# Performance work log

Measured on AMD Instinct MI355X. Metric: run time of the kernel, lower is better.

Reference implementation:

```python
import jax, jax.numpy as jnp
import numpy as np

N = 50000       # nodes
E = 800000      # edges (avg degree 16)
F_IN = 128      # num_node_features
H = 128         # hidden_dim
C = 16          # num_classes
G = 512         # graphs in batch


def setup_inputs() -> dict:
    key = jax.random.key(0)
    ks = jax.random.split(key, 12)
    x = jax.random.normal(ks[0], (N, F_IN), dtype=jnp.float32)
    edge_index = jax.random.randint(ks[1], (2, E), 0, N, dtype=jnp.int32)
    batch = jnp.sort(jax.random.randint(ks[2], (N,), 0, G, dtype=jnp.int32))
    def lin(k, fan_in, shape):
        bound = 1.0 / np.sqrt(fan_in)
        return jax.random.uniform(k, shape, jnp.float32, -bound, bound)
    # SAGEConv1: lin_l (aggr, with bias), lin_r (root, no bias)
    w1l = lin(ks[3], F_IN, (F_IN, H)); b1 = lin(ks[4], F_IN, (H,))
    w1r = lin(ks[5], F_IN, (F_IN, H))
    # SAGEConv2
    w2l = lin(ks[6], H, (H, H)); b2 = lin(ks[7], H, (H,))
    w2r = lin(ks[8], H, (H, H))
    # final fc
    wf = lin(ks[9], H, (H, C)); bf = lin(ks[10], H, (C,))
    return {"x": x, "edge_index": edge_index, "batch": batch,
            "w1l": w1l, "b1": b1, "w1r": w1r,
            "w2l": w2l, "b2": b2, "w2r": w2r,
            "wf": wf, "bf": bf}


def _sage_conv(x, src, dst, wl, bl, wr):
    # mean-aggregate source-node features at destination nodes
    msg_sum = jax.ops.segment_sum(x[src], dst, num_segments=N)      # [N, d]
    cnt = jax.ops.segment_sum(jnp.ones((src.shape[0], 1), x.dtype), dst,
                              num_segments=N)                        # [N, 1]
    aggr = msg_sum / jnp.maximum(cnt, 1.0)
    return aggr @ wl + bl + x @ wr


def reference(x, edge_index, batch, w1l, b1, w1r, w2l, b2, w2r, wf, bf):
    src, dst = edge_index[0], edge_index[1]
    h = jax.nn.relu(_sage_conv(x, src, dst, w1l, b1, w1r))
    # dropout(p=0.5) is identity at inference
    h = jax.nn.relu(_sage_conv(h, src, dst, w2l, b2, w2r))
    # global_mean_pool over graph ids
    gsum = jax.ops.segment_sum(h, batch, num_segments=G)             # [G, H]
    gcnt = jax.ops.segment_sum(jnp.ones((N, 1), h.dtype), batch,
                               num_segments=G)                        # [G, 1]
    g = gsum / jnp.maximum(gcnt, 1.0)
    logits = g @ wf + bf
    return jax.nn.log_softmax(logits, axis=1)
```

## Files before the change

### kernel.cpp

```cpp
#include <hip/hip_runtime.h>
#include <hip/hip_bf16.h>
#include <math.h>


#define FDIM 128

typedef __attribute__((ext_vector_type(8))) short bf16x8;
typedef __attribute__((ext_vector_type(4))) float f32x4;

__device__ inline unsigned short f2bf(float f) {
    union { float f; unsigned u; } v; v.f = f;
    unsigned r = v.u + 0x7fff + ((v.u >> 16) & 1);
    return (unsigned short)(r >> 16);
}
__device__ inline float bf2f(unsigned short b) {
    union { unsigned u; float f; } v; v.u = ((unsigned)b) << 16;
    return v.f;
}

__global__ void deg_rank_k(const int* __restrict__ dst, int* __restrict__ deg,
                           int* __restrict__ rank, int nE) {
    int e = blockIdx.x * blockDim.x + threadIdx.x;
    if (e < nE) rank[e] = atomicAdd(&deg[dst[e]], 1);
}

__global__ __launch_bounds__(256) void scan1_k(const int* __restrict__ deg,
                                               int* __restrict__ rowstart,
                                               int* __restrict__ bsum, int n) {
    __shared__ int s[256];
    int tid = threadIdx.x;
    int i = blockIdx.x * 256 + tid;
    int v = (i < n) ? deg[i] : 0;
    s[tid] = v;
    __syncthreads();
    for (int off = 1; off < 256; off <<= 1) {
        int t = (tid >= off) ? s[tid - off] : 0;
        __syncthreads();
        s[tid] += t;
        __syncthreads();
    }
    if (i < n) rowstart[i] = s[tid] - v;
    if (tid == 255) bsum[blockIdx.x] = s[255];
}

__global__ __launch_bounds__(256) void scan2_k(int* __restrict__ bsum, int nb) {
    __shared__ int s[256];
    int tid = threadIdx.x;
    int v = (tid < nb) ? bsum[tid] : 0;
    s[tid] = v;
    __syncthreads();
    for (int off = 1; off < 256; off <<= 1) {
        int t = (tid >= off) ? s[tid - off] : 0;
        __syncthreads();
        s[tid] += t;
        __syncthreads();
    }
    if (tid < nb) bsum[tid] = s[tid] - v;
}

__global__ void addoff_k(int* __restrict__ rowstart, const int* __restrict__ bsum, int n) {
    int i = blockIdx.x * blockDim.x + threadIdx.x;
    if (i < n) rowstart[i] += bsum[blockIdx.x];
}

__global__ __launch_bounds__(256) void fill_swz_k(
        const int* __restrict__ src, const int* __restrict__ dst,
        const int* __restrict__ rowstart, const int* __restrict__ rank,
        int* __restrict__ csr, int nE, int rngSize) {
    int cls = blockIdx.x & 7;
    int lo = cls * rngSize, hi = lo + rngSize;
    int nb = gridDim.x >> 3;
    int bi = blockIdx.x >> 3;
    for (int e = bi * 256 + threadIdx.x; e < nE; e += nb * 256) {
        int d = dst[e];
        if (d >= lo && d < hi)
            csr[rowstart[d] + rank[e]] = src[e];
    }
}

__global__ void cvt_bf16_k(const float* __restrict__ in, unsigned short* __restrict__ outp,
                           int n4) {
    int i = blockIdx.x * blockDim.x + threadIdx.x;
    if (i >= n4) return;
    float4 v = ((const float4*)in)[i];
    ushort4 o;
    o.x = f2bf(v.x); o.y = f2bf(v.y); o.z = f2bf(v.z); o.w = f2bf(v.w);
    ((ushort4*)outp)[i] = o;
}

__global__ __launch_bounds__(256) void pack_w_k(const float* __restrict__ wl,
                                                const float* __restrict__ wr,
                                                unsigned short* __restrict__ wp) {
    int t = blockIdx.x * 256 + threadIdx.x;
    int lane = t & 63, s = (t >> 6) & 7, nt = t >> 9;
    int kbase = s * 32 + ((lane >> 4) * 8);
    int c = nt * 16 + (lane & 15);
    ushort4 lo, hi;
    unsigned short tmp[8];
    #pragma unroll
    for (int j = 0; j < 8; ++j) {
        int k = kbase + j;
        float w = (k < 128) ? wl[k * 128 + c] : wr[(k - 128) * 128 + c];
        tmp[j] = f2bf(w);
    }
    lo.x = tmp[0]; lo.y = tmp[1]; lo.z = tmp[2]; lo.w = tmp[3];
    hi.x = tmp[4]; hi.y = tmp[5]; hi.z = tmp[6]; hi.w = tmp[7];
    ((ushort4*)wp)[t * 2 + 0] = lo;
    ((ushort4*)wp)[t * 2 + 1] = hi;
}

__global__ __launch_bounds__(256) void gather_mean_k(
        const uint2* __restrict__ feat,
        const int* __restrict__ csr, const int* __restrict__ rowstart,
        const int* __restrict__ deg, uint2* __restrict__ outr, int n) {
    int node = blockIdx.x * 4 + (threadIdx.x >> 6);
    if (node >= n) return;
    int lane = threadIdx.x & 63;
    int h = lane >> 5;
    int hl = lane & 31;
    int s0 = rowstart[node], dc = deg[node];

    float a0 = 0.f, a1 = 0.f, a2 = 0.f, a3 = 0.f;
    for (int base = 0; base < dc; base += 16) {
        uint2 w[8];
        #pragma unroll
        for (int k = 0; k < 8; ++k) {
            int e = base + 2 * k + h;
            int idx = (e < dc) ? csr[s0 + e] : 0;
            w[k] = feat[(size_t)idx * 32 + hl];
        }
        #pragma unroll
        for (int k = 0; k < 8; ++k) {
            int e = base + 2 * k + h;
            if (e >= dc) { w[k].x = 0; w[k].y = 0; }
            a0 += bf2f((unsigned short)(w[k].x & 0xffff));
            a1 += bf2f((unsigned short)(w[k].x >> 16));
            a2 += bf2f((unsigned short)(w[k].y & 0xffff));
            a3 += bf2f((unsigned short)(w[k].y >> 16));
        }
    }
    a0 += __shfl_xor(a0, 32, 64);
    a1 += __shfl_xor(a1, 32, 64);
    a2 += __shfl_xor(a2, 32, 64);
    a3 += __shfl_xor(a3, 32, 64);

    if (h == 0) {
        float inv = (dc > 0) ? 1.0f / (float)dc : 0.0f;
        uint2 o;
        o.x = ((unsigned)f2bf(a1 * inv) << 16) | (unsigned)f2bf(a0 * inv);
        o.y = ((unsigned)f2bf(a3 * inv) << 16) | (unsigned)f2bf(a2 * inv);
        outr[(size_t)node * 32 + hl] = o;
    }
}

__global__ __launch_bounds__(256) void gemm_mfma_k(
        const unsigned short* __restrict__ A,
        const unsigned short* __restrict__ R,
        const unsigned short* __restrict__ wp,
        const float* __restrict__ bias,
        unsigned short* __restrict__ outp,
        int n) {
    int tid = threadIdx.x;
    int wave = tid >> 6, lane = tid & 63;
    int rowTile = blockIdx.x * 64 + wave * 16;
    int lrow = lane & 15, lk = lane >> 4;

    int arow = rowTile + lrow;
    if (arow >= n) arow = n - 1;

    bf16x8 a[8];
    const unsigned short* abase = A + (size_t)arow * FDIM + lk * 8;
    const unsigned short* rbase = R + (size_t)arow * FDIM + lk * 8;
    #pragma unroll
    for (int s = 0; s < 4; ++s) a[s] = *(const bf16x8*)(abase + s * 32);
    #pragma unroll
    for (int s = 0; s < 4; ++s) a[4 + s] = *(const bf16x8*)(rbase + s * 32);

    const bf16x8* bp = (const bf16x8*)wp;
    int ocol = lane & 15;
    int orow0 = rowTile + (lane >> 4) * 4;

    #pragma unroll
    for (int nt = 0; nt < 8; ++nt) {
        float bv = bias[nt * 16 + ocol];
        f32x4 acc = {bv, bv, bv, bv};
        #pragma unroll
        for (int s = 0; s < 8; ++s) {
            bf16x8 b = bp[(nt * 8 + s) * 64 + lane];
            acc = __builtin_amdgcn_mfma_f32_16x16x32_bf16(a[s], b, acc, 0, 0, 0);
        }
        #pragma unroll
        for (int r = 0; r < 4; ++r) {
            int orow = orow0 + r;
            if (orow < n) {
                float v = fmaxf(acc[r], 0.0f);
                outp[(size_t)orow * FDIM + nt * 16 + ocol] = f2bf(v);
            }
        }
    }
}

__global__ __launch_bounds__(256) void pool_seg_k(
        const unsigned short* __restrict__ h,
        const int* __restrict__ batch,
        float* __restrict__ gsum, int* __restrict__ gcnt, int nN) {
    __shared__ int bw[64];
    __shared__ float red[8][32][4];
    int base = blockIdx.x * 64;
    if (base >= nN) return;
    int tid = threadIdx.x;
    int rg = tid >> 5, cs = tid & 31;
    int cnt = min(64, nN - base);
    if (tid < 64) bw[tid] = batch[min(base + tid, nN - 1)];
    __syncthreads();
    int g0 = bw[0], g1 = bw[cnt - 1];

    for (int g = g0; g <= g1; ++g) {
        int s = 0;
        while (s < cnt && bw[s] < g) ++s;
        int e = s;
        while (e < cnt && bw[e] == g) ++e;

        float a0 = 0.f, a1 = 0.f, a2 = 0.f, a3 = 0.f;
        for (int i = s + rg; i < e; i += 8) {
            uint2 v = ((const uint2*)(h + (size_t)(base + i) * FDIM))[cs];
            a0 += bf2f((unsigned short)(v.x & 0xffff));
            a1 += bf2f((unsigned short)(v.x >> 16));
            a2 += bf2f((unsigned short)(v.y & 0xffff));
            a3 += bf2f((unsigned short)(v.y >> 16));
        }
        red[rg][cs][0] = a0; red[rg][cs][1] = a1;
        red[rg][cs][2] = a2; red[rg][cs][3] = a3;
        __syncthreads();
        if (rg == 0 && e > s) {
            #pragma unroll
            for (int r = 1; r < 8; ++r) {
                a0 += red[r][cs][0]; a1 += red[r][cs][1];
                a2 += red[r][cs][2]; a3 += red[r][cs][3];
            }
            float* go = gsum + (size_t)g * FDIM + cs * 4;
            atomicAdd(go + 0, a0);
            atomicAdd(go + 1, a1);
            atomicAdd(go + 2, a2);
            atomicAdd(go + 3, a3);
            if (cs == 0) atomicAdd(&gcnt[g], e - s);
        }
        __syncthreads();
    }
}

__global__ __launch_bounds__(128) void head_k(const float* __restrict__ gsum,
                                              const int* __restrict__ gcnt,
                                              const float* __restrict__ wf,
                                              const float* __restrict__ bf,
                                              float* __restrict__ out, int nG) {
    int g = blockIdx.x;
    if (g >= nG) return;
    __shared__ float row[FDIM];
    int tid = threadIdx.x;
    float inv = 1.0f / fmaxf((float)gcnt[g], 1.0f);
    row[tid] = gsum[(size_t)g * FDIM + tid] * inv;
    __syncthreads();

    float logit = -1e30f;
    if (tid < 16) {
        logit = bf[tid];
        for (int k = 0; k < FDIM; ++k) logit += row[k] * wf[k * 16 + tid];
    }
    float m = logit;
    for (int off = 8; off >= 1; off >>= 1) m = fmaxf(m, __shfl_xor(m, off, 64));
    float ev = (tid < 16) ? expf(logit - m) : 0.0f;
    float sum = ev;
    for (int off = 8; off >= 1; off >>= 1) sum += __shfl_xor(sum, off, 64);
    if (tid < 16) out[(size_t)g * 16 + tid] = logit - m - logf(sum);
}

extern "C" void kernel_launch(void* const* d_in, const int* in_sizes, int n_in,
                              void* d_out, int out_size, void* d_ws, size_t ws_size,
                              hipStream_t stream) {
    const float* x    = (const float*)d_in[0];
    const int*   ei   = (const int*)d_in[1];
    const int*   batch= (const int*)d_in[2];
    const float* w1l  = (const float*)d_in[3];
    const float* b1   = (const float*)d_in[4];
    const float* w1r  = (const float*)d_in[5];
    const float* w2l  = (const float*)d_in[6];
    const float* b2   = (const float*)d_in[7];
    const float* w2r  = (const float*)d_in[8];
    const float* wf   = (const float*)d_in[9];
    const float* bf   = (const float*)d_in[10];
    float* out = (float*)d_out;

    const int N = in_sizes[0] / FDIM;
    const int E = in_sizes[1] / 2;
    const int G = out_size / 16;
    const int* src = ei;
    const int* dst = ei + E;
    const int NB = (N + 255) / 256;

    char* ws = (char*)d_ws;
    size_t off = 0;
    auto alloc = [&](size_t bytes) { void* p = ws + off; off = (off + bytes + 255) & ~(size_t)255; return p; };
    unsigned short* xb   = (unsigned short*)alloc((size_t)N * FDIM * 2);
    unsigned short* aggr = (unsigned short*)alloc((size_t)N * FDIM * 2);
    unsigned short* h1   = (unsigned short*)alloc((size_t)N * FDIM * 2);
    unsigned short* wp1  = (unsigned short*)alloc(8 * 8 * 64 * 8 * 2);
    unsigned short* wp2  = (unsigned short*)alloc(8 * 8 * 64 * 8 * 2);
    int* deg      = (int*)alloc((size_t)N * sizeof(int));
    int* rowstart = (int*)alloc((size_t)N * sizeof(int));
    int* bsum     = (int*)alloc(256 * sizeof(int));
    int* csr      = (int*)alloc((size_t)E * sizeof(int));
    int* rank     = (int*)alloc((size_t)E * sizeof(int));
    float* gsum   = (float*)alloc((size_t)G * FDIM * sizeof(float));
    int*   gcnt   = (int*)alloc((size_t)G * sizeof(int));
    unsigned short* h2 = xb;

    hipMemsetAsync(deg, 0, (size_t)N * sizeof(int), stream);
    deg_rank_k<<<(E + 255) / 256, 256, 0, stream>>>(dst, deg, rank, E);
    scan1_k<<<NB, 256, 0, stream>>>(deg, rowstart, bsum, N);
    scan2_k<<<1, 256, 0, stream>>>(bsum, NB);
    addoff_k<<<NB, 256, 0, stream>>>(rowstart, bsum, N);
    {
        int rngSize = (N + 7) / 8;
        fill_swz_k<<<2048, 256, 0, stream>>>(src, dst, rowstart, rank, csr, E, rngSize);
    }

    cvt_bf16_k<<<(N * FDIM / 4 + 255) / 256, 256, 0, stream>>>(x, xb, N * FDIM / 4);
    pack_w_k<<<16, 256, 0, stream>>>(w1l, w1r, wp1);
    pack_w_k<<<16, 256, 0, stream>>>(w2l, w2r, wp2);
    hipMemsetAsync(gsum, 0, (size_t)G * FDIM * sizeof(float), stream);
    hipMemsetAsync(gcnt, 0, (size_t)G * sizeof(int), stream);

    gather_mean_k<<<(N + 3) / 4, 256, 0, stream>>>((const uint2*)xb, csr, rowstart, deg,
                                                   (uint2*)aggr, N);
    gemm_mfma_k<<<(N + 63) / 64, 256, 0, stream>>>(aggr, xb, wp1, b1, h1, N);

    gather_mean_k<<<(N + 3) / 4, 256, 0, stream>>>((const uint2*)h1, csr, rowstart, deg,
                                                   (uint2*)aggr, N);
    gemm_mfma_k<<<(N + 63) / 64, 256, 0, stream>>>(aggr, h1, wp2, b2, h2, N);

    pool_seg_k<<<(N + 63) / 64, 256, 0, stream>>>(h2, batch, gsum, gcnt, N);
    head_k<<<G, 128, 0, stream>>>(gsum, gcnt, wf, bf, out, G);
}
```

Measured before the change: 213.0 us.

## Fuse neighbor mean-gather into MFMA GEMM per layer and merge prep kernels

Each SAGE layer now gathers neighbor means for 16 rows per wave into shared memory, then runs the MFMA GEMM from there. This removes the aggr intermediate buffer write/read and one launch per layer. Separately, degree counting, x-to-bf16 conversion and weight packing are merged into one multi-role prep kernel. The trade-off is fewer waves in flight during the latency-bound gather (782 blocks, each wave processing two nodes at a time), which could hurt latency hiding.

Result: slower. 232.0 us (+8.9%).

```diff
diff --git a/kernel.cpp b/kernel.cpp
--- a/kernel.cpp
+++ b/kernel.cpp
@@ -18,10 +18,48 @@
     return v.f;
 }
 
-__global__ void deg_rank_k(const int* __restrict__ dst, int* __restrict__ deg,
-                           int* __restrict__ rank, int nE) {
-    int e = blockIdx.x * blockDim.x + threadIdx.x;
-    if (e < nE) rank[e] = atomicAdd(&deg[dst[e]], 1);
+__global__ __launch_bounds__(256) void prep_k(
+        const int* __restrict__ dst, int* __restrict__ deg, int* __restrict__ rank, int nE,
+        const float* __restrict__ x, unsigned short* __restrict__ xb, int n4,
+        const float* __restrict__ w1l, const float* __restrict__ w1r,
+        unsigned short* __restrict__ wp1,
+        const float* __restrict__ w2l, const float* __restrict__ w2r,
+        unsigned short* __restrict__ wp2,
+        int nbE, int nbC) {
+    int bid = blockIdx.x, tid = threadIdx.x;
+    if (bid < nbE) {
+        int e = bid * 256 + tid;
+        if (e < nE) rank[e] = atomicAdd(&deg[dst[e]], 1);
+    } else if (bid < nbE + nbC) {
+        int i = (bid - nbE) * 256 + tid;
+        if (i < n4) {
+            float4 v = ((const float4*)x)[i];
+            ushort4 o;
+            o.x = f2bf(v.x); o.y = f2bf(v.y); o.z = f2bf(v.z); o.w = f2bf(v.w);
+            ((ushort4*)xb)[i] = o;
+        }
+    } else {
+        int pb = bid - nbE - nbC;
+        const float* wl = (pb < 16) ? w1l : w2l;
+        const float* wr = (pb < 16) ? w1r : w2r;
+        unsigned short* wp = (pb < 16) ? wp1 : wp2;
+        int t = (pb & 15) * 256 + tid;
+        int lane = t & 63, s = (t >> 6) & 7, nt = t >> 9;
+        int kbase = s * 32 + ((lane >> 4) * 8);
+        int c = nt * 16 + (lane & 15);
+        unsigned short tmp[8];
+        #pragma unroll
+        for (int j = 0; j < 8; ++j) {
+            int k = kbase + j;
+            float w = (k < 128) ? wl[k * 128 + c] : wr[(k - 128) * 128 + c];
+            tmp[j] = f2bf(w);
+        }
+        ushort4 lo, hi;
+        lo.x = tmp[0]; lo.y = tmp[1]; lo.z = tmp[2]; lo.w = tmp[3];
+        hi.x = tmp[4]; hi.y = tmp[5]; hi.z = tmp[6]; hi.w = tmp[7];
+        ((ushort4*)wp)[t * 2 + 0] = lo;
+        ((ushort4*)wp)[t * 2 + 1] = hi;
+    }
 }
 
 __global__ __launch_bounds__(256) void scan1_k(const int* __restrict__ deg,
@@ -78,103 +116,85 @@
     }
 }
 
-__global__ void cvt_bf16_k(const float* __restrict__ in, unsigned short* __restrict__ outp,
-                           int n4) {
-    int i = blockIdx.x * blockDim.x + threadIdx.x;
-    if (i >= n4) return;
-    float4 v = ((const float4*)in)[i];
-    ushort4 o;
-    o.x = f2bf(v.x); o.y = f2bf(v.y); o.z = f2bf(v.z); o.w = f2bf(v.w);
-    ((ushort4*)outp)[i] = o;
-}
-
-__global__ __launch_bounds__(256) void pack_w_k(const float* __restrict__ wl,
-                                                const float* __restrict__ wr,
-                                                unsigned short* __restrict__ wp) {
-    int t = blockIdx.x * 256 + threadIdx.x;
-    int lane = t & 63, s = (t >> 6) & 7, nt = t >> 9;
-    int kbase = s * 32 + ((lane >> 4) * 8);
-    int c = nt * 16 + (lane & 15);
-    ushort4 lo, hi;
-    unsigned short tmp[8];
-    #pragma unroll
-    for (int j = 0; j < 8; ++j) {
-        int k = kbase + j;
-        float w = (k < 128) ? wl[k * 128 + c] : wr[(k - 128) * 128 + c];
-        tmp[j] = f2bf(w);
-    }
-    lo.x = tmp[0]; lo.y = tmp[1]; lo.z = tmp[2]; lo.w = tmp[3];
-    hi.x = tmp[4]; hi.y = tmp[5]; hi.z = tmp[6]; hi.w = tmp[7];
-    ((ushort4*)wp)[t * 2 + 0] = lo;
-    ((ushort4*)wp)[t * 2 + 1] = hi;
-}
-
-__global__ __launch_bounds__(256) void gather_mean_k(
+__global__ __launch_bounds__(256) void sage_layer_k(
         const uint2* __restrict__ feat,
+        const unsigned short* __restrict__ root,
         const int* __restrict__ csr, const int* __restrict__ rowstart,
-        const int* __restrict__ deg, uint2* __restrict__ outr, int n) {
-    int node = blockIdx.x * 4 + (threadIdx.x >> 6);
-    if (node >= n) return;
-    int lane = threadIdx.x & 63;
-    int h = lane >> 5;
-    int hl = lane & 31;
-    int s0 = rowstart[node], dc = deg[node];
-
-    float a0 = 0.f, a1 = 0.f, a2 = 0.f, a3 = 0.f;
-    for (int base = 0; base < dc; base += 16) {
-        uint2 w[8];
-        #pragma unroll
-        for (int k = 0; k < 8; ++k) {
-            int e = base + 2 * k + h;
-            int idx = (e < dc) ? csr[s0 + e] : 0;
-            w[k] = feat[(size_t)idx * 32 + hl];
-        }
-        #pragma unroll
-        for (int k = 0; k < 8; ++k) {
-            int e = base + 2 * k + h;
-            if (e >= dc) { w[k].x = 0; w[k].y = 0; }
-            a0 += bf2f((unsigned short)(w[k].x & 0xffff));
-            a1 += bf2f((unsigned short)(w[k].x >> 16));
-            a2 += bf2f((unsigned short)(w[k].y & 0xffff));
-            a3 += bf2f((unsigned short)(w[k].y >> 16));
-        }
-    }
-    a0 += __shfl_xor(a0, 32, 64);
-    a1 += __shfl_xor(a1, 32, 64);
-    a2 += __shfl_xor(a2, 32, 64);
-    a3 += __shfl_xor(a3, 32, 64);
-
-    if (h == 0) {
-        float inv = (dc > 0) ? 1.0f / (float)dc : 0.0f;
-        uint2 o;
-        o.x = ((unsigned)f2bf(a1 * inv) << 16) | (unsigned)f2bf(a0 * inv);
-        o.y = ((unsigned)f2bf(a3 * inv) << 16) | (unsigned)f2bf(a2 * inv);
-        outr[(size_t)node * 32 + hl] = o;
-    }
-}
-
-__global__ __launch_bounds__(256) void gemm_mfma_k(
-        const unsigned short* __restrict__ A,
-        const unsigned short* __restrict__ R,
+        const int* __restrict__ deg,
         const unsigned short* __restrict__ wp,
         const float* __restrict__ bias,
         unsigned short* __restrict__ outp,
         int n) {
+    __shared__ __align__(16) unsigned short arow[4][16][136];
     int tid = threadIdx.x;
     int wave = tid >> 6, lane = tid & 63;
     int rowTile = blockIdx.x * 64 + wave * 16;
+    int h = lane >> 5, hl = lane & 31;
+
+    for (int r = 0; r < 16; r += 2) {
+        int nA = rowTile + r, nB = rowTile + r + 1;
+        int sA = 0, dA = 0, sB = 0, dB = 0;
+        if (nA < n) { sA = rowstart[nA]; dA = deg[nA]; }
+        if (nB < n) { sB = rowstart[nB]; dB = deg[nB]; }
+        float a0 = 0.f, a1 = 0.f, a2 = 0.f, a3 = 0.f;
+        float b0 = 0.f, b1 = 0.f, b2 = 0.f, b3 = 0.f;
+        int dmax = max(dA, dB);
+        for (int be = 0; be < dmax; be += 16) {
+            uint2 wA[8], wB[8];
+            #pragma unroll
+            for (int k = 0; k < 8; ++k) {
+                int e = be + 2 * k + h;
+                int iA = (e < dA) ? csr[sA + e] : -1;
+                int iB = (e < dB) ? csr[sB + e] : -1;
+                wA[k] = feat[(size_t)max(iA, 0) * 32 + hl];
+                wB[k] = feat[(size_t)max(iB, 0) * 32 + hl];
+                if (iA < 0) { wA[k].x = 0; wA[k].y = 0; }
+                if (iB < 0) { wB[k].x = 0; wB[k].y = 0; }
+            }
+            #pragma unroll
+            for (int k = 0; k < 8; ++k) {
+                a0 += bf2f((unsigned short)(wA[k].x & 0xffff));
+                a1 += bf2f((unsigned short)(wA[k].x >> 16));
+                a2 += bf2f((unsigned short)(wA[k].y & 0xffff));
+                a3 += bf2f((unsigned short)(wA[k].y >> 16));
+                b0 += bf2f((unsigned short)(wB[k].x & 0xffff));
+                b1 += bf2f((unsigned short)(wB[k].x >> 16));
+                b2 += bf2f((unsigned short)(wB[k].y & 0xffff));
+                b3 += bf2f((unsigned short)(wB[k].y >> 16));
+            }
+        }
+        a0 += __shfl_xor(a0, 32, 64);
+        a1 += __shfl_xor(a1, 32, 64);
+        a2 += __shfl_xor(a2, 32, 64);
+        a3 += __shfl_xor(a3, 32, 64);
+        b0 += __shfl_xor(b0, 32, 64);
+        b1 += __shfl_xor(b1, 32, 64);
+        b2 += __shfl_xor(b2, 32, 64);
+        b3 += __shfl_xor(b3, 32, 64);
+        if (h == 0) {
+            float invA = (dA > 0) ? 1.0f / (float)dA : 0.0f;
+            float invB = (dB > 0) ? 1.0f / (float)dB : 0.0f;
+            uint2 oA, oB;
+            oA.x = ((unsigned)f2bf(a1 * invA) << 16) | (unsigned)f2bf(a0 * invA);
+            oA.y = ((unsigned)f2bf(a3 * invA) << 16) | (unsigned)f2bf(a2 * invA);
+            oB.x = ((unsigned)f2bf(b1 * invB) << 16) | (unsigned)f2bf(b0 * invB);
+            oB.y = ((unsigned)f2bf(b3 * invB) << 16) | (unsigned)f2bf(b2 * invB);
+            *(uint2*)&arow[wave][r][hl * 4] = oA;
+            *(uint2*)&arow[wave][r + 1][hl * 4] = oB;
+        }
+    }
+
     int lrow = lane & 15, lk = lane >> 4;
-
-    int arow = rowTile + lrow;
-    if (arow >= n) arow = n - 1;
-
     bf16x8 a[8];
-    const unsigned short* abase = A + (size_t)arow * FDIM + lk * 8;
-    const unsigned short* rbase = R + (size_t)arow * FDIM + lk * 8;
     #pragma unroll
-    for (int s = 0; s < 4; ++s) a[s] = *(const bf16x8*)(abase + s * 32);
+    for (int s = 0; s < 4; ++s)
+        a[s] = *(const bf16x8*)&arow[wave][lrow][s * 32 + lk * 8];
+    int grow = rowTile + lrow;
+    if (grow >= n) grow = n - 1;
+    const unsigned short* rbase = root + (size_t)grow * FDIM + lk * 8;
     #pragma unroll
-    for (int s = 0; s < 4; ++s) a[4 + s] = *(const bf16x8*)(rbase + s * 32);
+    for (int s = 0; s < 4; ++s)
+        a[4 + s] = *(const bf16x8*)(rbase + s * 32);
 
     const bf16x8* bp = (const bf16x8*)wp;
     int ocol = lane & 15;
@@ -302,7 +322,6 @@
     size_t off = 0;
     auto alloc = [&](size_t bytes) { void* p = ws + off; off = (off + bytes + 255) & ~(size_t)255; return p; };
     unsigned short* xb   = (unsigned short*)alloc((size_t)N * FDIM * 2);
-    unsigned short* aggr = (unsigned short*)alloc((size_t)N * FDIM * 2);
     unsigned short* h1   = (unsigned short*)alloc((size_t)N * FDIM * 2);
     unsigned short* wp1  = (unsigned short*)alloc(8 * 8 * 64 * 8 * 2);
     unsigned short* wp2  = (unsigned short*)alloc(8 * 8 * 64 * 8 * 2);
@@ -316,7 +335,16 @@
     unsigned short* h2 = xb;
 
     hipMemsetAsync(deg, 0, (size_t)N * sizeof(int), stream);
-    deg_rank_k<<<(E + 255) / 256, 256, 0, stream>>>(dst, deg, rank, E);
+    hipMemsetAsync(gsum, 0, (size_t)G * FDIM * sizeof(float), stream);
+    hipMemsetAsync(gcnt, 0, (size_t)G * sizeof(int), stream);
+
+    const int nbE = (E + 255) / 256;
+    const int nbC = (N * FDIM / 4 + 255) / 256;
+    prep_k<<<nbE + nbC + 32, 256, 0, stream>>>(dst, deg, rank, E,
+                                               x, xb, N * FDIM / 4,
+                                               w1l, w1r, wp1, w2l, w2r, wp2,
+                                               nbE, nbC);
+
     scan1_k<<<NB, 256, 0, stream>>>(deg, rowstart, bsum, N);
     scan2_k<<<1, 256, 0, stream>>>(bsum, NB);
     addoff_k<<<NB, 256, 0, stream>>>(rowstart, bsum, N);
@@ -325,19 +353,10 @@
         fill_swz_k<<<2048, 256, 0, stream>>>(src, dst, rowstart, rank, csr, E, rngSize);
     }
 
-    cvt_bf16_k<<<(N * FDIM / 4 + 255) / 256, 256, 0, stream>>>(x, xb, N * FDIM / 4);
-    pack_w_k<<<16, 256, 0, stream>>>(w1l, w1r, wp1);
-    pack_w_k<<<16, 256, 0, stream>>>(w2l, w2r, wp2);
-    hipMemsetAsync(gsum, 0, (size_t)G * FDIM * sizeof(float), stream);
-    hipMemsetAsync(gcnt, 0, (size_t)G * sizeof(int), stream);
-
-    gather_mean_k<<<(N + 3) / 4, 256, 0, stream>>>((const uint2*)xb, csr, rowstart, deg,
-                                                   (uint2*)aggr, N);
-    gemm_mfma_k<<<(N + 63) / 64, 256, 0, stream>>>(aggr, xb, wp1, b1, h1, N);
-
-    gather_mean_k<<<(N + 3) / 4, 256, 0, stream>>>((const uint2*)h1, csr, rowstart, deg,
-                                                   (uint2*)aggr, N);
-    gemm_mfma_k<<<(N + 63) / 64, 256, 0, stream>>>(aggr, h1, wp2, b2, h2, N);
+    sage_layer_k<<<(N + 63) / 64, 256, 0, stream>>>((const uint2*)xb, xb, csr, rowstart,
+                                                    deg, wp1, b1, h1, N);
+    sage_layer_k<<<(N + 63) / 64, 256, 0, stream>>>((const uint2*)h1, h1, csr, rowstart,
+                                                    deg, wp2, b2, h2, N);
 
     pool_seg_k<<<(N + 63) / 64, 256, 0, stream>>>(h2, batch, gsum, gcnt, N);
     head_k<<<G, 128, 0, stream>>>(gsum, gcnt, wf, bf, out, G);
```
